# Performance work log

Hardware: AMD Instinct MI355X
Metric: run time of the kernel (lower is better)

Reference implementation:

```python
import jax, jax.numpy as jnp
import numpy as np

DIM = 1024
N_HEADS = 16
HEAD_DIM = DIM // N_HEADS
SCALE = HEAD_DIM ** -0.5


def setup_inputs() -> dict:
    key = jax.random.key(0)
    kx, kq, kk, kv = jax.random.split(key, 4)
    x = jax.random.normal(kx, (2, 2048, DIM), dtype=jnp.float32)
    bv_q = jax.random.normal(kq, (N_HEADS, HEAD_DIM), dtype=jnp.float32) * 0.02
    bv_k = jax.random.normal(kk, (N_HEADS, HEAD_DIM), dtype=jnp.float32) * 0.02
    bv_v = jax.random.normal(kv, (N_HEADS, HEAD_DIM), dtype=jnp.float32) * 0.02
    return {"x": x, "bv_q": bv_q, "bv_k": bv_k, "bv_v": bv_v}


def reference(x, bv_q, bv_k, bv_v):
    B, T, D = x.shape
    H, HD = N_HEADS, HEAD_DIM
    x_h = x.reshape(B, T, H, HD)
    # sign-gated Q/K/V (sign of binding vectors; elementwise +/-1 gating)
    Q = x_h * jnp.sign(bv_q)  # [B,T,H,HD]
    K = x_h * jnp.sign(bv_k)
    V = x_h * jnp.sign(bv_v)
    # causal scores, sigmoid gating (no softmax)
    scores = jnp.einsum('bqhd,bkhd->bhqk', Q, K) * SCALE  # [B,H,T,T]
    causal = jnp.tril(jnp.ones((T, T), dtype=bool))
    attn = jnp.where(causal, jax.nn.sigmoid(scores * 4.0), 0.0)
    out = jnp.einsum('bhqk,bkhd->bqhd', attn, V)  # [B,T,H,HD]
    return out.reshape(B, T, D)
```

## Files before the change

kernel.cpp:

```cpp
#include <hip/hip_runtime.h>
#include <hip/hip_bf16.h>
#include <stdint.h>

#define DIM 1024
#define T_LEN 2048
#define NB 2
#define NH 16
#define HD 64
#define NQT 32

typedef float f32x2 __attribute__((ext_vector_type(2)));
typedef float f32x4 __attribute__((ext_vector_type(4)));
typedef float f32x16 __attribute__((ext_vector_type(16)));
typedef __bf16 bf16x8 __attribute__((ext_vector_type(8)));
typedef __bf16 bf16x2 __attribute__((ext_vector_type(2)));
typedef unsigned int u32;
typedef unsigned int u32x4 __attribute__((ext_vector_type(4)));

__device__ __forceinline__ float sgnf(float v) {
    return (v > 0.f) ? 1.f : ((v < 0.f) ? -1.f : 0.f);
}

__device__ __forceinline__ u32 pack2(float p0, float p1) {
    bf16x2 t = {(__bf16)p0, (__bf16)p1};
    return __builtin_bit_cast(u32, t);
}

__device__ __forceinline__ void gload16(const __bf16* g, __bf16* l) {
    __builtin_amdgcn_global_load_lds(
        (__attribute__((address_space(1))) void*)g,
        (__attribute__((address_space(3))) void*)l,
        16, 0, 0);
}

__global__ __launch_bounds__(256) void prep_kernel(
    const float* __restrict__ x, const float* __restrict__ bvv,
    __bf16* __restrict__ xb, __bf16* __restrict__ xt)
{
    __shared__ __align__(16) __bf16 tile[64][72];

    const int bid = blockIdx.x;
    const int h = bid & 15, tmp = bid >> 4, tt = tmp & 31, b = tmp >> 5;
    const int tid = threadIdx.x;
    const int r = tid >> 2, c0 = (tid & 3) * 16;

    const size_t rowbase = ((size_t)(b * T_LEN + tt * 64 + r)) * DIM + h * HD + c0;
    const float* xp = x + rowbase;

    __bf16 v[16];
    #pragma unroll
    for (int i = 0; i < 16; i += 4) {
        f32x4 f = *(const f32x4*)(xp + i);
        #pragma unroll
        for (int j = 0; j < 4; ++j) v[i + j] = (__bf16)f[j];
    }
    bf16x8 s0, s1;
    #pragma unroll
    for (int j = 0; j < 8; ++j) { s0[j] = v[j]; s1[j] = v[8 + j]; }
    *(bf16x8*)(xb + rowbase)     = s0;
    *(bf16x8*)(xb + rowbase + 8) = s1;
    *(bf16x8*)&tile[r][c0]     = s0;
    *(bf16x8*)&tile[r][c0 + 8] = s1;

    __syncthreads();

    const int d = tid >> 2, t0c = (tid & 3) * 16;
    const float g = sgnf(bvv[h * HD + d]);
    __bf16 ov[16];
    #pragma unroll
    for (int i = 0; i < 16; ++i) ov[i] = (__bf16)((float)tile[t0c + i][d] * g);
    bf16x8 o0, o1;
    #pragma unroll
    for (int j = 0; j < 8; ++j) { o0[j] = ov[j]; o1[j] = ov[8 + j]; }
    const size_t obase = ((size_t)((b * NH + h) * HD + d)) * T_LEN + tt * 64 + t0c;
    *(bf16x8*)(xt + obase)     = o0;
    *(bf16x8*)(xt + obase + 8) = o1;
}

__global__ __launch_bounds__(256, 4) void mba_main(
    const __bf16* __restrict__ xb, const __bf16* __restrict__ xt,
    const float* __restrict__ bvq, const float* __restrict__ bvk,
    float* __restrict__ out)
{
    __shared__ __align__(16) __bf16 Kb[2][64][64];
    __shared__ __align__(16) __bf16 Vb[2][64][64];

    const int bid = blockIdx.x;
    const int u = bid >> 5;
    const int jj = u >> 3, aa = u & 7;
    const int qt = 8 * jj + ((jj & 1) ? (7 - aa) : aa);
    const int bh = bid & 31;
    const int b = bh >> 4, h = bh & 15;
    const int q0 = qt * 64;

    const int tid = threadIdx.x;
    const int w = tid >> 6, l = tid & 63;
    const int c = l & 31, hi = l >> 5;
    const int qh = w & 1, sh = w >> 1;

    const size_t xb_bh = (size_t)b * T_LEN * DIM + h * HD;
    const size_t xt_bh = (size_t)((b * NH + h) * HD) * T_LEN;

    const int rr = l >> 3;
    const int sw = ((l & 7) ^ rr) << 3;

    auto STAGE_K = [&](int buf, int kvt) {
        const int kv0s = kvt * 64;
        #pragma unroll
        for (int pt = 0; pt < 2; ++pt) {
            const int r0 = w * 8 + pt * 32;
            gload16(xb + xb_bh + (size_t)(kv0s + r0 + rr) * DIM + sw, &Kb[buf][r0][0]);
        }
    };
    auto STAGE_V = [&](int buf, int kvt) {
        const int kv0s = kvt * 64;
        #pragma unroll
        for (int pt = 0; pt < 2; ++pt) {
            const int r0 = w * 8 + pt * 32;
            gload16(xt + xt_bh + (size_t)(r0 + rr) * T_LEN + kv0s + sw, &Vb[buf][r0][0]);
        }
    };

    STAGE_K(0, 0);
    STAGE_V(0, 0);

    bf16x8 qa[4];
    {
        const float* bq = bvq + h * HD;
        const float* bk = bvk + h * HD;
        const int qrow = q0 + qh * 32 + c;
        #pragma unroll
        for (int m = 0; m < 4; ++m) {
            const int d0 = m * 16 + hi * 8;
            bf16x8 va = *(const bf16x8*)(xb + xb_bh + (size_t)qrow * DIM + d0);
            #pragma unroll
            for (int j = 0; j < 8; ++j) {
                float f = sgnf(bq[d0 + j]) * sgnf(bk[d0 + j]);
                qa[m][j] = (__bf16)((float)va[j] * f);
            }
        }
    }

    f32x16 o[2];
    #pragma unroll
    for (int nd = 0; nd < 2; ++nd)
        #pragma unroll
        for (int i = 0; i < 16; ++i) o[nd][i] = 0.f;

    const int krow = sh * 32 + c;
    const int swz = (c & 7) << 4;

    auto bodyfn = [&](int t, int pb) {
        const bool diag = (t == qt);
        asm volatile("s_waitcnt vmcnt(0)" ::: "memory");
        __builtin_amdgcn_sched_barrier(0);
        __builtin_amdgcn_s_barrier();
        __builtin_amdgcn_sched_barrier(0);

        if (t + 1 <= qt) {
            STAGE_V(pb ^ 1, t + 1);
            STAGE_K(pb ^ 1, t + 1);
        }
        __builtin_amdgcn_sched_barrier(0);

        f32x16 ss;
        #pragma unroll
        for (int i = 0; i < 16; ++i) ss[i] = 0.f;
        __builtin_amdgcn_s_setprio(1);
        #pragma unroll
        for (int m = 0; m < 4; ++m) {
            bf16x8 kf = *(const bf16x8*)((const char*)&Kb[pb][krow][0]
                          + ((m * 32 + hi * 16) ^ swz));
            ss = __builtin_amdgcn_mfma_f32_32x32x16_bf16(kf, qa[m], ss, 0, 0, 0);
        }
        __builtin_amdgcn_s_setprio(0);

        u32 W[8];
        #pragma unroll
        for (int i = 0; i < 8; ++i) {
            const int r0 = 2 * i;
            const int sl = (r0 & 3) + 8 * (r0 >> 2) + 4 * hi;
            f32x2 z = {ss[r0], ss[r0 + 1]};
            z = z * (-0.72134752f);
            f32x2 e = {__builtin_amdgcn_exp2f(z.x), __builtin_amdgcn_exp2f(z.y)};
            e = e + 1.0f;
            float p0 = __builtin_amdgcn_rcpf(e.x);
            float p1 = __builtin_amdgcn_rcpf(e.y);
            if (diag) {
                const int sg = sh * 32 + sl;
                const int qg = qh * 32 + c;
                if (sg > qg)     p0 = 0.f;
                if (sg + 1 > qg) p1 = 0.f;
            }
            W[i] = pack2(p0, p1);
        }

        asm volatile("v_permlane32_swap_b32 %0, %1" : "+v"(W[0]), "+v"(W[2]));
        asm volatile("v_permlane32_swap_b32 %0, %1" : "+v"(W[1]), "+v"(W[3]));
        asm volatile("v_permlane32_swap_b32 %0, %1" : "+v"(W[4]), "+v"(W[6]));
        asm volatile("v_permlane32_swap_b32 %0, %1" : "+v"(W[5]), "+v"(W[7]));
        bf16x8 pa[2];
        pa[0] = __builtin_bit_cast(bf16x8, (u32x4){W[0], W[1], W[2], W[3]});
        pa[1] = __builtin_bit_cast(bf16x8, (u32x4){W[4], W[5], W[6], W[7]});

        __builtin_amdgcn_s_setprio(1);
        #pragma unroll
        for (int m = 0; m < 2; ++m) {
            #pragma unroll
            for (int nd = 0; nd < 2; ++nd) {
                bf16x8 vf = *(const bf16x8*)((const char*)&Vb[pb][nd * 32 + c][0]
                              + ((sh * 64 + m * 32 + hi * 16) ^ swz));
                o[nd] = __builtin_amdgcn_mfma_f32_32x32x16_bf16(pa[m], vf, o[nd], 0, 0, 0);
            }
        }
        __builtin_amdgcn_s_setprio(0);
    };

    for (int t = 0; t <= qt; t += 2) {
        bodyfn(t, 0);
        if (t + 1 <= qt) bodyfn(t + 1, 1);
    }

    __syncthreads();
    float (*osc)[64] = (float(*)[64]) & Kb[0][0][0];

    if (sh == 1) {
        #pragma unroll
        for (int r = 0; r < 16; ++r) {
            const int qloc = (r & 3) + 8 * (r >> 2) + 4 * hi;
            osc[qh * 32 + qloc][c]      = o[0][r];
            osc[qh * 32 + qloc][32 + c] = o[1][r];
        }
    }
    __syncthreads();
    if (sh == 0) {
        #pragma unroll
        for (int r = 0; r < 16; ++r) {
            const int qloc = (r & 3) + 8 * (r >> 2) + 4 * hi;
            const size_t row = (size_t)(b * T_LEN + q0 + qh * 32 + qloc) * DIM + h * HD;
            out[row + c]      = o[0][r] + osc[qh * 32 + qloc][c];
            out[row + 32 + c] = o[1][r] + osc[qh * 32 + qloc][32 + c];
        }
    }
}

__global__ __launch_bounds__(256) void mba_fallback(
    const float* __restrict__ x,
    const float* __restrict__ bvq,
    const float* __restrict__ bvk,
    const float* __restrict__ bvv,
    float* __restrict__ out)
{
    __shared__ __align__(16) __bf16 Kb[64][72];
    __shared__ __align__(16) __bf16 Vt[HD][72];
    __shared__ __align__(16) __bf16 Pb[4][16][72];

    const int bid = blockIdx.x;
    const int qt  = (NQT - 1) - (bid & (NQT - 1));
    const int bh  = bid >> 5;
    const int b   = bh >> 4;
    const int h   = bh & 15;

    const int tid = threadIdx.x;
    const int w   = tid >> 6;
    const int l   = tid & 63;
    const int lq  = l & 15;
    const int lh  = l >> 4;

    const int  q0    = qt * 64;
    const long xbase = ((long)b * T_LEN) * DIM + h * HD;

    bf16x8 qa[2];
    {
        const int   qrow = q0 + w * 16 + lq;
        const float* qp  = x + xbase + (long)qrow * DIM + lh * 8;
        const float* gp  = bvq + h * HD + lh * 8;
        #pragma unroll
        for (int ks = 0; ks < 2; ++ks)
            #pragma unroll
            for (int j = 0; j < 8; ++j)
                qa[ks][j] = (__bf16)(qp[ks * 32 + j] * sgnf(gp[ks * 32 + j]));
    }

    f32x4 o[4];
    #pragma unroll
    for (int n = 0; n < 4; ++n) o[n] = (f32x4){0.f, 0.f, 0.f, 0.f};

    const int r_st = tid >> 2;
    const int c0   = (tid & 3) * 16;
    const float* gk = bvk + h * HD + c0;
    const float* gv = bvv + h * HD + c0;

    for (int kvt = 0; kvt <= qt; ++kvt) {
        const int kv0 = kvt * 64;
        __syncthreads();
        {
            const float* kp = x + xbase + (long)(kv0 + r_st) * DIM + c0;
            __bf16 kb[16];
            #pragma unroll
            for (int i = 0; i < 16; ++i) kb[i] = (__bf16)(kp[i] * sgnf(gk[i]));
            *(bf16x8*)&Kb[r_st][c0]     = *(bf16x8*)&kb[0];
            *(bf16x8*)&Kb[r_st][c0 + 8] = *(bf16x8*)&kb[8];
            #pragma unroll
            for (int i = 0; i < 16; ++i)
                Vt[c0 + i][r_st] = (__bf16)(kp[i] * sgnf(gv[i]));
        }
        __syncthreads();

        f32x4 s[4];
        #pragma unroll
        for (int n = 0; n < 4; ++n) s[n] = (f32x4){0.f, 0.f, 0.f, 0.f};
        #pragma unroll
        for (int ks = 0; ks < 2; ++ks)
            #pragma unroll
            for (int n = 0; n < 4; ++n) {
                bf16x8 kf = *(const bf16x8*)&Kb[n * 16 + lq][ks * 32 + lh * 8];
                s[n] = __builtin_amdgcn_mfma_f32_16x16x32_bf16(qa[ks], kf, s[n], 0, 0, 0);
            }

        const bool diag = (kvt == qt);
        #pragma unroll
        for (int n = 0; n < 4; ++n)
            #pragma unroll
            for (int j = 0; j < 4; ++j) {
                float sc = s[n][j];
                float p = __builtin_amdgcn_rcpf(
                              1.f + __builtin_amdgcn_exp2f(-0.72134752f * sc));
                if (diag && (n * 16 + lq) > (w * 16 + lh * 4 + j)) p = 0.f;
                Pb[w][lh * 4 + j][n * 16 + lq] = (__bf16)p;
            }

        #pragma unroll
        for (int ks = 0; ks < 2; ++ks) {
            bf16x8 pf = *(const bf16x8*)&Pb[w][lq][ks * 32 + lh * 8];
            #pragma unroll
            for (int n = 0; n < 4; ++n) {
                bf16x8 vf = *(const bf16x8*)&Vt[n * 16 + lq][ks * 32 + lh * 8];
                o[n] = __builtin_amdgcn_mfma_f32_16x16x32_bf16(pf, vf, o[n], 0, 0, 0);
            }
        }
    }

    float* op = out + ((long)b * T_LEN + q0 + w * 16) * DIM + h * HD;
    #pragma unroll
    for (int n = 0; n < 4; ++n)
        #pragma unroll
        for (int j = 0; j < 4; ++j)
            op[(long)(lh * 4 + j) * DIM + n * 16 + lq] = o[n][j];
}

extern "C" void kernel_launch(void* const* d_in, const int* in_sizes, int n_in,
                              void* d_out, int out_size, void* d_ws, size_t ws_size,
                              hipStream_t stream) {
    (void)in_sizes; (void)n_in; (void)out_size;
    const float* x   = (const float*)d_in[0];
    const float* bvq = (const float*)d_in[1];
    const float* bvk = (const float*)d_in[2];
    const float* bvv = (const float*)d_in[3];
    float* out = (float*)d_out;

    const size_t XB_BYTES = (size_t)NB * T_LEN * DIM * sizeof(__bf16);
    const size_t XT_BYTES = XB_BYTES;

    if (ws_size < XB_BYTES + XT_BYTES) {
        mba_fallback<<<NB * NH * NQT, 256, 0, stream>>>(x, bvq, bvk, bvv, out);
        return;
    }

    __bf16* xb = (__bf16*)d_ws;
    __bf16* xt = xb + (size_t)NB * T_LEN * DIM;

    prep_kernel<<<NB * NQT * NH, 256, 0, stream>>>(x, bvv, xb, xt);
    mba_main<<<NB * NH * NQT, 256, 0, stream>>>(xb, xt, bvq, bvk, out);
}
```

Before: 54.10 us.

## Triple-buffer K tiles and prefetch K two tiles ahead with partial vmcnt waits

K tiles move to a three-slot ring and are prefetched two iterations ahead, while V stays double-buffered one ahead. Each iteration now waits with vmcnt(2) instead of draining all loads, so the newest K prefetch can stay in flight across the barrier. The loop is unrolled by six with compile-time buffer indices. The change also removes the s_setprio hints and uses inline v_cvt_pk_bf16_f32 for packing. It costs extra LDS (another 8KB K buffer), which may affect occupancy at 4 blocks per CU, and relies on correct vmcnt accounting.

```diff
diff --git a/kernel.cpp b/kernel.cpp
--- a/kernel.cpp
+++ b/kernel.cpp
@@ -17,13 +17,10 @@
 typedef unsigned int u32;
 typedef unsigned int u32x4 __attribute__((ext_vector_type(4)));
 
+template <int N> struct ICT { static constexpr int v = N; };
+
 __device__ __forceinline__ float sgnf(float v) {
     return (v > 0.f) ? 1.f : ((v < 0.f) ? -1.f : 0.f);
-}
-
-__device__ __forceinline__ u32 pack2(float p0, float p1) {
-    bf16x2 t = {(__bf16)p0, (__bf16)p1};
-    return __builtin_bit_cast(u32, t);
 }
 
 __device__ __forceinline__ void gload16(const __bf16* g, __bf16* l) {
@@ -82,7 +79,7 @@
     const float* __restrict__ bvq, const float* __restrict__ bvk,
     float* __restrict__ out)
 {
-    __shared__ __align__(16) __bf16 Kb[2][64][64];
+    __shared__ __align__(16) __bf16 Kb[3][64][64];
     __shared__ __align__(16) __bf16 Vb[2][64][64];
 
     const int bid = blockIdx.x;
@@ -104,25 +101,21 @@
     const int rr = l >> 3;
     const int sw = ((l & 7) ^ rr) << 3;
 
-    auto STAGE_K = [&](int buf, int kvt) {
-        const int kv0s = kvt * 64;
-        #pragma unroll
-        for (int pt = 0; pt < 2; ++pt) {
-            const int r0 = w * 8 + pt * 32;
-            gload16(xb + xb_bh + (size_t)(kv0s + r0 + rr) * DIM + sw, &Kb[buf][r0][0]);
-        }
-    };
-    auto STAGE_V = [&](int buf, int kvt) {
-        const int kv0s = kvt * 64;
-        #pragma unroll
-        for (int pt = 0; pt < 2; ++pt) {
-            const int r0 = w * 8 + pt * 32;
-            gload16(xt + xt_bh + (size_t)(r0 + rr) * T_LEN + kv0s + sw, &Vb[buf][r0][0]);
-        }
-    };
-
-    STAGE_K(0, 0);
-    STAGE_V(0, 0);
+    const __bf16* kbase = xb + xb_bh + (size_t)(w * 8 + rr) * DIM + sw;
+    const __bf16* vbase = xt + xt_bh + (size_t)(w * 8 + rr) * T_LEN + sw;
+    const size_t KROW32 = (size_t)32 * DIM;
+    const size_t VROW32 = (size_t)32 * T_LEN;
+
+    gload16(kbase,          &Kb[0][w * 8][0]);
+    gload16(kbase + KROW32, &Kb[0][w * 8 + 32][0]);
+    gload16(vbase,          &Vb[0][w * 8][0]);
+    gload16(vbase + VROW32, &Vb[0][w * 8 + 32][0]);
+    if (qt >= 1) {
+        gload16(kbase + (size_t)64 * DIM,          &Kb[1][w * 8][0]);
+        gload16(kbase + (size_t)64 * DIM + KROW32, &Kb[1][w * 8 + 32][0]);
+    }
+    const __bf16* kst = kbase + (size_t)128 * DIM;
+    const __bf16* vst = vbase + 64;
 
     bf16x8 qa[4];
     {
@@ -150,75 +143,87 @@
     const int krow = sh * 32 + c;
     const int swz = (c & 7) << 4;
 
-    auto bodyfn = [&](int t, int pb) {
-        const bool diag = (t == qt);
-        asm volatile("s_waitcnt vmcnt(0)" ::: "memory");
+    auto body = [&](int tt, auto kbT, auto vbT) {
+        constexpr int KB = decltype(kbT)::v;
+        constexpr int VB = decltype(vbT)::v;
+        const bool last = (tt == qt);
+        if (last) { asm volatile("s_waitcnt vmcnt(0)" ::: "memory"); }
+        else      { asm volatile("s_waitcnt vmcnt(2)" ::: "memory"); }
         __builtin_amdgcn_sched_barrier(0);
         __builtin_amdgcn_s_barrier();
         __builtin_amdgcn_sched_barrier(0);
 
-        if (t + 1 <= qt) {
-            STAGE_V(pb ^ 1, t + 1);
-            STAGE_K(pb ^ 1, t + 1);
+        if (tt + 1 <= qt) {
+            gload16(vst,          &Vb[VB ^ 1][w * 8][0]);
+            gload16(vst + VROW32, &Vb[VB ^ 1][w * 8 + 32][0]);
+            vst += 64;
         }
         __builtin_amdgcn_sched_barrier(0);
+        if (tt + 2 <= qt) {
+            gload16(kst,          &Kb[(KB + 2) % 3][w * 8][0]);
+            gload16(kst + KROW32, &Kb[(KB + 2) % 3][w * 8 + 32][0]);
+            kst += (size_t)64 * DIM;
+        }
+        __builtin_amdgcn_sched_barrier(0);
 
         f32x16 ss;
         #pragma unroll
         for (int i = 0; i < 16; ++i) ss[i] = 0.f;
-        __builtin_amdgcn_s_setprio(1);
         #pragma unroll
         for (int m = 0; m < 4; ++m) {
-            bf16x8 kf = *(const bf16x8*)((const char*)&Kb[pb][krow][0]
+            bf16x8 kf = *(const bf16x8*)((const char*)&Kb[KB][krow][0]
                           + ((m * 32 + hi * 16) ^ swz));
             ss = __builtin_amdgcn_mfma_f32_32x32x16_bf16(kf, qa[m], ss, 0, 0, 0);
         }
-        __builtin_amdgcn_s_setprio(0);
 
         u32 W[8];
         #pragma unroll
         for (int i = 0; i < 8; ++i) {
             const int r0 = 2 * i;
-            const int sl = (r0 & 3) + 8 * (r0 >> 2) + 4 * hi;
-            f32x2 z = {ss[r0], ss[r0 + 1]};
+            f32x2 z; z.x = ss[r0]; z.y = ss[r0 + 1];
             z = z * (-0.72134752f);
-            f32x2 e = {__builtin_amdgcn_exp2f(z.x), __builtin_amdgcn_exp2f(z.y)};
+            f32x2 e;
+            e.x = __builtin_amdgcn_exp2f(z.x);
+            e.y = __builtin_amdgcn_exp2f(z.y);
             e = e + 1.0f;
             float p0 = __builtin_amdgcn_rcpf(e.x);
             float p1 = __builtin_amdgcn_rcpf(e.y);
-            if (diag) {
+            if (last) {
+                const int sl = (r0 & 3) + 8 * (r0 >> 2) + 4 * hi;
                 const int sg = sh * 32 + sl;
                 const int qg = qh * 32 + c;
                 if (sg > qg)     p0 = 0.f;
                 if (sg + 1 > qg) p1 = 0.f;
             }
-            W[i] = pack2(p0, p1);
+            asm("v_cvt_pk_bf16_f32 %0, %1, %2" : "=v"(W[i]) : "v"(p0), "v"(p1));
         }
 
         asm volatile("v_permlane32_swap_b32 %0, %1" : "+v"(W[0]), "+v"(W[2]));
         asm volatile("v_permlane32_swap_b32 %0, %1" : "+v"(W[1]), "+v"(W[3]));
         asm volatile("v_permlane32_swap_b32 %0, %1" : "+v"(W[4]), "+v"(W[6]));
         asm volatile("v_permlane32_swap_b32 %0, %1" : "+v"(W[5]), "+v"(W[7]));
-        bf16x8 pa[2];
-        pa[0] = __builtin_bit_cast(bf16x8, (u32x4){W[0], W[1], W[2], W[3]});
-        pa[1] = __builtin_bit_cast(bf16x8, (u32x4){W[4], W[5], W[6], W[7]});
-
-        __builtin_amdgcn_s_setprio(1);
+        bf16x8 pa0 = __builtin_bit_cast(bf16x8, (u32x4){W[0], W[1], W[2], W[3]});
+        bf16x8 pa1 = __builtin_bit_cast(bf16x8, (u32x4){W[4], W[5], W[6], W[7]});
+
         #pragma unroll
         for (int m = 0; m < 2; ++m) {
+            const bf16x8 paM = m ? pa1 : pa0;
             #pragma unroll
             for (int nd = 0; nd < 2; ++nd) {
-                bf16x8 vf = *(const bf16x8*)((const char*)&Vb[pb][nd * 32 + c][0]
+                bf16x8 vf = *(const bf16x8*)((const char*)&Vb[VB][nd * 32 + c][0]
                               + ((sh * 64 + m * 32 + hi * 16) ^ swz));
-                o[nd] = __builtin_amdgcn_mfma_f32_32x32x16_bf16(pa[m], vf, o[nd], 0, 0, 0);
-            }
-        }
-        __builtin_amdgcn_s_setprio(0);
+                o[nd] = __builtin_amdgcn_mfma_f32_32x32x16_bf16(paM, vf, o[nd], 0, 0, 0);
+            }
+        }
     };
 
-    for (int t = 0; t <= qt; t += 2) {
-        bodyfn(t, 0);
-        if (t + 1 <= qt) bodyfn(t + 1, 1);
+    for (int t = 0; t <= qt; t += 6) {
+        body(t, ICT<0>{}, ICT<0>{});
+        if (t + 1 <= qt) body(t + 1, ICT<1>{}, ICT<1>{});
+        if (t + 2 <= qt) body(t + 2, ICT<2>{}, ICT<0>{});
+        if (t + 3 <= qt) body(t + 3, ICT<0>{}, ICT<1>{});
+        if (t + 4 <= qt) body(t + 4, ICT<1>{}, ICT<0>{});
+        if (t + 5 <= qt) body(t + 5, ICT<2>{}, ICT<1>{});
     }
 
     __syncthreads();
```

After: 48.34 us. -10.6%, faster.
